# Kernel tuning notes

Hardware: AMD Instinct MI355X
Metric: run time of the kernel (lower is better)

The kernel has to match this reference:

```python
import jax, jax.numpy as jnp
import numpy as np

CODEBOOK_DIM = 256
HIDDEN_DIM = 512
OUT_CHANNELS = 1
NUM_NODES = 16384
NUM_INPUT_ROWS = 12288


def setup_inputs() -> dict:
    key = jax.random.key(0)
    k0, k1, k2, k3, k4 = jax.random.split(key, 5)
    x = jax.random.normal(k0, (NUM_INPUT_ROWS, CODEBOOK_DIM), dtype=jnp.float32)
    # GCNConv params: linear weight (no bias in lin) + additive bias after aggregation
    W1 = jax.random.normal(k1, (CODEBOOK_DIM, HIDDEN_DIM), dtype=jnp.float32) * (1.0 / np.sqrt(CODEBOOK_DIM))
    b1 = jax.random.normal(k2, (HIDDEN_DIM,), dtype=jnp.float32) * 0.01
    W2 = jax.random.normal(k3, (HIDDEN_DIM, OUT_CHANNELS), dtype=jnp.float32) * (1.0 / np.sqrt(HIDDEN_DIM))
    b2 = jax.random.normal(k4, (OUT_CHANNELS,), dtype=jnp.float32) * 0.01
    return {"x": x, "W1": W1, "b1": b1, "W2": W2, "b2": b2, "num_nodes": NUM_NODES}


def _gcn_complete(h, W, b, n):
    # GCNConv on a complete graph (no self-loop edges in edge_index, but
    # GCNConv adds self-loops): A_hat = D^{-1/2}(A+I)D^{-1/2} = J/N since
    # A+I is all-ones and every degree is N. So aggregation == column mean
    # broadcast to every node.
    hw = h @ W                                   # [N, d_out]
    agg = jnp.mean(hw, axis=0, keepdims=True)    # [1, d_out]
    return jnp.broadcast_to(agg, (n, W.shape[1])) + b


def reference(x, W1, b1, W2, b2, num_nodes):
    n = num_nodes
    missing = n - x.shape[0]
    x = jnp.concatenate([x, jnp.zeros((missing, x.shape[1]), x.dtype)], axis=0)  # [N, codebook_dim]
    h = jax.nn.relu(_gcn_complete(x, W1, b1, n))   # [N, hidden]
    out = jax.nn.relu(_gcn_complete(h, W2, b2, n)) # [N, out_channels]
    return out
```

## Files before the change

### kernel.cpp

```cpp
#include <hip/hip_runtime.h>

#define NROWS   12288
#define NCOLS   256
#define HID     512
#define NNODES  16384
#define NB      128
#define ITERS   (NROWS / (4 * NB))
#define NTAIL   8
#define TAG32   0x9E3779B9u
#define TAG64   ((unsigned long long)TAG32 << 32)

#define WS_FLOATS_NEEDED 53264

__global__ __launch_bounds__(256) void colsum_partial_128(const float* __restrict__ x,
                                                          float* __restrict__ wsA) {
    const int t    = threadIdx.x;
    const int c4   = t & 63;
    const int rofs = t >> 6;
    const int bid  = blockIdx.x;
    const float4* __restrict__ x4 = (const float4*)x;

    float4 acc = make_float4(0.f, 0.f, 0.f, 0.f);
    #pragma unroll
    for (int k = 0; k < ITERS; ++k) {
        const int r = bid * 4 + rofs + k * (4 * NB);
        float4 v = x4[r * 64 + c4];
        acc.x += v.x; acc.y += v.y; acc.z += v.z; acc.w += v.w;
    }

    __shared__ float4 s[256];
    s[t] = acc;
    __syncthreads();
    if (t < 64) {
        float4 a = s[t], b = s[t + 64], c = s[t + 128], d = s[t + 192];
        float4 r;
        r.x = a.x + b.x + c.x + d.x;
        r.y = a.y + b.y + c.y + d.y;
        r.z = a.z + b.z + c.z + d.z;
        r.w = a.w + b.w + c.w + d.w;
        ((float4*)wsA)[bid * 64 + t] = r;
    }
}

__global__ __launch_bounds__(512) void tail_kernel(const float* __restrict__ wsA,
                                                   const float* __restrict__ W1,
                                                   const float* __restrict__ b1,
                                                   const float* __restrict__ W2,
                                                   const float* __restrict__ b2,
                                                   unsigned long long* __restrict__ flagS,
                                                   float* __restrict__ out) {
    __shared__ float4 tmp4[512];
    __shared__ float  colmean[NCOLS];
    __shared__ float  part[512];
    __shared__ float  sval;

    const int t   = threadIdx.x;
    const int b   = blockIdx.x;
    const int w   = t >> 6;
    const int l   = t & 63;
    const int myt = b * 64 + l;

    float w1r[32];
    #pragma unroll
    for (int j = 0; j < 32; ++j)
        w1r[j] = W1[(w * 32 + j) * HID + myt];
    float b1r = 0.f, w2r = 0.f, b2r = 0.f;
    if (t < 64) { b1r = b1[myt]; w2r = W2[myt]; b2r = b2[0]; }

    {
        const float4* __restrict__ wsA4 = (const float4*)wsA;
        float4 acc = make_float4(0.f, 0.f, 0.f, 0.f);
        #pragma unroll
        for (int j = 0; j < NB / 8; ++j) {
            float4 v = wsA4[(w * (NB / 8) + j) * 64 + l];
            acc.x += v.x; acc.y += v.y; acc.z += v.z; acc.w += v.w;
        }
        tmp4[t] = acc;
        __syncthreads();
        if (t < 64) {
            float4 a = tmp4[t];
            #pragma unroll
            for (int g = 1; g < 8; ++g) {
                float4 v = tmp4[g * 64 + t];
                a.x += v.x; a.y += v.y; a.z += v.z; a.w += v.w;
            }
            const float inv = 1.0f / (float)NNODES;
            a.x *= inv; a.y *= inv; a.z *= inv; a.w *= inv;
            ((float4*)colmean)[t] = a;
        }
        __syncthreads();
    }

    {
        float pa = 0.f;
        #pragma unroll
        for (int j = 0; j < 32; ++j)
            pa = fmaf(colmean[w * 32 + j], w1r[j], pa);
        part[t] = pa;
        __syncthreads();

        if (t < 64) {
            float hs = b1r;
            #pragma unroll
            for (int g = 0; g < 8; ++g)
                hs += part[g * 64 + t];
            const float h = fmaxf(hs, 0.0f);

            float p = h * w2r;
            #pragma unroll
            for (int off = 32; off > 0; off >>= 1)
                p += __shfl_down(p, off, 64);
            if (t == 0)
                __hip_atomic_store(&flagS[b],
                                   TAG64 | (unsigned long long)__float_as_uint(p),
                                   __ATOMIC_RELAXED, __HIP_MEMORY_SCOPE_AGENT);
        }
    }

    float f = 0.f;
    if (t < NTAIL) {
        unsigned long long v;
        while (((v = __hip_atomic_load(&flagS[t], __ATOMIC_RELAXED,
                                       __HIP_MEMORY_SCOPE_AGENT)) >> 32) != TAG32)
            __builtin_amdgcn_s_sleep(1);
        f = __uint_as_float((unsigned int)v);
    }

    if (t < 64) {
        float ssum = 0.f;
        #pragma unroll
        for (int i = 0; i < NTAIL; ++i)
            ssum += __shfl(f, i, 64);
        if (t == 0) sval = fmaxf(b2r + ssum, 0.0f);
    }
    __syncthreads();

    const float v = sval;
    ((float4*)out)[b * 512 + t] = make_float4(v, v, v, v);
}

__global__ __launch_bounds__(256) void colsum_dyn(const float* __restrict__ x,
                                                  float* __restrict__ wsA, int nb) {
    const int t = threadIdx.x, c4 = t & 63, rofs = t >> 6, bid = blockIdx.x;
    const float4* __restrict__ x4 = (const float4*)x;
    float4 acc = make_float4(0.f, 0.f, 0.f, 0.f);
    for (int r = bid * 4 + rofs; r < NROWS; r += 4 * nb) {
        float4 v = x4[r * 64 + c4];
        acc.x += v.x; acc.y += v.y; acc.z += v.z; acc.w += v.w;
    }
    __shared__ float4 s[256];
    s[t] = acc; __syncthreads();
    if (t < 64) {
        float4 a = s[t], b = s[t+64], c = s[t+128], d = s[t+192];
        float4 r; r.x=a.x+b.x+c.x+d.x; r.y=a.y+b.y+c.y+d.y;
        r.z=a.z+b.z+c.z+d.z; r.w=a.w+b.w+c.w+d.w;
        ((float4*)wsA)[bid * 64 + t] = r;
    }
}
__global__ __launch_bounds__(512) void hidden_dyn(const float* __restrict__ wsA,
                                                  const float* __restrict__ W1,
                                                  const float* __restrict__ b1,
                                                  const float* __restrict__ W2,
                                                  float* __restrict__ wsB, int nb) {
    __shared__ float4 tmp4[512];
    __shared__ float colmean[NCOLS];
    __shared__ float part[512];
    const int t = threadIdx.x, b = blockIdx.x;
    {
        const int c4 = t & 63, g = t >> 6, per = nb >> 3;
        const float4* __restrict__ w4 = (const float4*)wsA;
        float4 acc = make_float4(0.f, 0.f, 0.f, 0.f);
        for (int k = g * per; k < g * per + per; ++k) {
            float4 v = w4[k * 64 + c4];
            acc.x += v.x; acc.y += v.y; acc.z += v.z; acc.w += v.w;
        }
        tmp4[t] = acc; __syncthreads();
        if (t < 64) {
            float4 a = tmp4[t];
            for (int g2 = 1; g2 < 8; ++g2) {
                float4 v = tmp4[g2 * 64 + t];
                a.x += v.x; a.y += v.y; a.z += v.z; a.w += v.w;
            }
            const float inv = 1.0f / (float)NNODES;
            a.x *= inv; a.y *= inv; a.z *= inv; a.w *= inv;
            ((float4*)colmean)[t] = a;
        }
        __syncthreads();
    }
    const int w = t >> 6, l = t & 63, myt = b * 64 + l;
    float pa = 0.f;
    for (int c = w * 32; c < w * 32 + 32; ++c)
        pa = fmaf(colmean[c], W1[c * HID + myt], pa);
    part[t] = pa; __syncthreads();
    if (t < 64) {
        float hs = b1[myt];
        for (int g = 0; g < 8; ++g) hs += part[g * 64 + l];
        const float h = fmaxf(hs, 0.0f);
        float p = h * W2[myt];
        for (int off = 32; off > 0; off >>= 1) p += __shfl_down(p, off, 64);
        if (l == 0) wsB[b] = p;
    }
}
__global__ __launch_bounds__(256) void bcast_dyn(const float* __restrict__ wsB,
                                                 const float* __restrict__ b2,
                                                 float* __restrict__ out) {
    __shared__ float sval;
    if (threadIdx.x == 0) {
        float s = b2[0];
        for (int i = 0; i < 8; ++i) s += wsB[i];
        sval = fmaxf(s, 0.0f);
    }
    __syncthreads();
    const float v = sval;
    ((float4*)out)[blockIdx.x * 256 + threadIdx.x] = make_float4(v, v, v, v);
}

extern "C" void kernel_launch(void* const* d_in, const int* in_sizes, int n_in,
                              void* d_out, int out_size, void* d_ws, size_t ws_size,
                              hipStream_t stream) {
    const float* x  = (const float*)d_in[0];
    const float* W1 = (const float*)d_in[1];
    const float* b1 = (const float*)d_in[2];
    const float* W2 = (const float*)d_in[3];
    const float* b2 = (const float*)d_in[4];
    float* out = (float*)d_out;
    float* ws  = (float*)d_ws;

    if (ws_size >= (size_t)WS_FLOATS_NEEDED * sizeof(float)) {
        float*              wsA   = ws;
        unsigned long long* flagS = (unsigned long long*)(ws + 53248);
        colsum_partial_128<<<NB, 256, 0, stream>>>(x, wsA);
        tail_kernel<<<NTAIL, 512, 0, stream>>>(wsA, W1, b1, W2, b2, flagS, out);
    } else {
        int nb = (int)((ws_size / sizeof(float) - 8) / NCOLS);
        nb &= ~7; if (nb < 8) nb = 8;
        float* wsA = ws;
        float* wsB = ws + (size_t)nb * NCOLS;
        colsum_dyn<<<nb, 256, 0, stream>>>(x, wsA, nb);
        hidden_dyn<<<8, 512, 0, stream>>>(wsA, W1, b1, W2, wsB, nb);
        bcast_dyn<<<16, 256, 0, stream>>>(wsB, b2, out);
    }
}
```

Measured before the change: 14.63 us.

## Split partial-sum reduction across tail blocks and exchange via tagged flags

Each of the 8 tail blocks previously reduced all 128 partial column sums redundantly. Now each block reduces only its 16-partial slice and publishes the result as tagged 64-bit words in workspace. Every block then spin-waits on the other blocks' tagged values and combines them into the column mean. This cuts redundant global reads per block, but adds a cross-block spin-wait that relies on all 8 blocks being resident at once, and tag-based freshness that could in principle match stale workspace contents.

```diff
diff --git a/kernel.cpp b/kernel.cpp
--- a/kernel.cpp
+++ b/kernel.cpp
@@ -7,10 +7,11 @@
 #define NB      128
 #define ITERS   (NROWS / (4 * NB))
 #define NTAIL   8
-#define TAG32   0x9E3779B9u
+#define SLICE   (NB / NTAIL)
+#define TAG32   0xC2B2AE35u
 #define TAG64   ((unsigned long long)TAG32 << 32)
 
-#define WS_FLOATS_NEEDED 53264
+#define WS_FLOATS_NEEDED 61456
 
 __global__ __launch_bounds__(256) void colsum_partial_128(const float* __restrict__ x,
                                                           float* __restrict__ wsA) {
@@ -47,9 +48,11 @@
                                                    const float* __restrict__ b1,
                                                    const float* __restrict__ W2,
                                                    const float* __restrict__ b2,
+                                                   unsigned long long* __restrict__ flagP,
                                                    unsigned long long* __restrict__ flagS,
                                                    float* __restrict__ out) {
     __shared__ float4 tmp4[512];
+    __shared__ float  suball[NTAIL * NCOLS];
     __shared__ float  colmean[NCOLS];
     __shared__ float  part[512];
     __shared__ float  sval;
@@ -71,8 +74,8 @@
         const float4* __restrict__ wsA4 = (const float4*)wsA;
         float4 acc = make_float4(0.f, 0.f, 0.f, 0.f);
         #pragma unroll
-        for (int j = 0; j < NB / 8; ++j) {
-            float4 v = wsA4[(w * (NB / 8) + j) * 64 + l];
+        for (int k = 0; k < 2; ++k) {
+            float4 v = wsA4[(b * SLICE + w * 2 + k) * 64 + l];
             acc.x += v.x; acc.y += v.y; acc.z += v.z; acc.w += v.w;
         }
         tmp4[t] = acc;
@@ -84,12 +87,40 @@
                 float4 v = tmp4[g * 64 + t];
                 a.x += v.x; a.y += v.y; a.z += v.z; a.w += v.w;
             }
-            const float inv = 1.0f / (float)NNODES;
-            a.x *= inv; a.y *= inv; a.z *= inv; a.w *= inv;
-            ((float4*)colmean)[t] = a;
-        }
-        __syncthreads();
-    }
+            const int base = b * NCOLS + t * 4;
+            __hip_atomic_store(&flagP[base + 0],
+                               TAG64 | (unsigned long long)__float_as_uint(a.x),
+                               __ATOMIC_RELAXED, __HIP_MEMORY_SCOPE_AGENT);
+            __hip_atomic_store(&flagP[base + 1],
+                               TAG64 | (unsigned long long)__float_as_uint(a.y),
+                               __ATOMIC_RELAXED, __HIP_MEMORY_SCOPE_AGENT);
+            __hip_atomic_store(&flagP[base + 2],
+                               TAG64 | (unsigned long long)__float_as_uint(a.z),
+                               __ATOMIC_RELAXED, __HIP_MEMORY_SCOPE_AGENT);
+            __hip_atomic_store(&flagP[base + 3],
+                               TAG64 | (unsigned long long)__float_as_uint(a.w),
+                               __ATOMIC_RELAXED, __HIP_MEMORY_SCOPE_AGENT);
+        }
+    }
+
+    #pragma unroll
+    for (int i = 0; i < 4; ++i) {
+        const int idx = t * 4 + i;
+        unsigned long long v;
+        while (((v = __hip_atomic_load(&flagP[idx], __ATOMIC_RELAXED,
+                                       __HIP_MEMORY_SCOPE_AGENT)) >> 32) != TAG32)
+            __builtin_amdgcn_s_sleep(1);
+        suball[idx] = __uint_as_float((unsigned int)v);
+    }
+    __syncthreads();
+    if (t < NCOLS) {
+        float s = 0.f;
+        #pragma unroll
+        for (int g = 0; g < NTAIL; ++g)
+            s += suball[g * NCOLS + t];
+        colmean[t] = s * (1.0f / (float)NNODES);
+    }
+    __syncthreads();
 
     {
         float pa = 0.f;
@@ -228,9 +259,11 @@
 
     if (ws_size >= (size_t)WS_FLOATS_NEEDED * sizeof(float)) {
         float*              wsA   = ws;
-        unsigned long long* flagS = (unsigned long long*)(ws + 53248);
+        unsigned long long* flagP = (unsigned long long*)(ws + 57344);
+        unsigned long long* flagS = (unsigned long long*)(ws + 61440);
         colsum_partial_128<<<NB, 256, 0, stream>>>(x, wsA);
-        tail_kernel<<<NTAIL, 512, 0, stream>>>(wsA, W1, b1, W2, b2, flagS, out);
+        tail_kernel<<<NTAIL, 512, 0, stream>>>(wsA, W1, b1, W2, b2,
+                                               flagP, flagS, out);
     } else {
         int nb = (int)((ws_size / sizeof(float) - 8) / NCOLS);
         nb &= ~7; if (nb < 8) nb = 8;
```

Result: no change. 14.85 us (+1.5%).
